# Optimization experiments

Hardware: AMD Instinct MI355X
Metric: run time of the kernel (lower is better)

The kernel has to match this reference:

```python
import jax, jax.numpy as jnp
import numpy as np

B, D = 128, 64  # batch; channel == height == width == dim == 64 (hardcoded by the module)


def setup_inputs() -> dict:
    key = jax.random.key(0)
    kx, kc, kh, kw = jax.random.split(key, 4)
    x = jax.random.normal(kx, (B, D, D, D), dtype=jnp.float32)
    # Stacked 1x1 conv weights: [i (loop index), out_channels, in_channels]
    Wc = jax.random.normal(kc, (D, D, D), dtype=jnp.float32) * 0.1
    Wh = jax.random.normal(kh, (D, D, D), dtype=jnp.float32) * 0.1
    Ww = jax.random.normal(kw, (D, D, D), dtype=jnp.float32) * 0.1
    return {"x": x, "Wc": Wc, "Wh": Wh, "Ww": Ww}


def reference(x, Wc, Wh, Ww):
    # x: [b, c, h, w] with c == h == w == 64
    # Adaptive avg-pool to 1x1 on three permutations -> three [b, 64] vectors.
    c_vec = x.mean(axis=(2, 3))  # pool over (h, w): channel descriptor   [b, 64]
    h_vec = x.mean(axis=(1, 2))  # pool over (c, h): width descriptor    [b, 64]
    w_vec = x.mean(axis=(1, 3))  # pool over (c, w): height descriptor   [b, 64]

    # All 64 per-iteration 1x1 convs + sigmoid as one batched GEMM per branch.
    # Wc[i, o, j]: weight of the i-th conv; conv(C)[o] = sum_j Wc[i,o,j] * c_vec[b,j]
    fc = jax.nn.sigmoid(jnp.einsum('ioj,bj->bio', Wc, c_vec))  # [b, 64(i), 64]
    fh = jax.nn.sigmoid(jnp.einsum('ioj,bj->bio', Wh, h_vec))  # [b, 64(i), 64]
    fw = jax.nn.sigmoid(jnp.einsum('ioj,bj->bio', Ww, w_vec))  # [b, 64(i), 64]

    # recon: bmm(bmm(C, H), W) == outer product fc_i (x) fh_i (x) fw_i, summed over i.
    LR = jnp.einsum('bic,bip,biq->bcpq', fc, fh, fw)  # [b, 64, 64, 64]
    return LR
```

## Files before the change

### kernel.cpp

```cpp
#include <hip/hip_runtime.h>
#include <hip/hip_bf16.h>


#define NB 128

typedef __attribute__((ext_vector_type(8))) short bf16x8;
typedef __attribute__((ext_vector_type(4))) float f32x4;

__device__ __forceinline__ float bf2f(short s) {
    return __uint_as_float(((unsigned)(unsigned short)s) << 16);
}
__device__ __forceinline__ unsigned packbf2(float a, float b) {
    unsigned ua = __float_as_uint(a); ua += 0x7fffu + ((ua >> 16) & 1u);
    unsigned ub = __float_as_uint(b); ub += 0x7fffu + ((ub >> 16) & 1u);
    return (ua >> 16) | (ub & 0xffff0000u);
}
__device__ __forceinline__ unsigned short f2bf(float f) {
    unsigned u = __float_as_uint(f); u += 0x7fffu + ((u >> 16) & 1u);
    return (unsigned short)(u >> 16);
}

__global__ __launch_bounds__(256) void pool_kernel(const float* __restrict__ x,
                                                   float* __restrict__ cvecT,
                                                   float* __restrict__ hv_part,
                                                   float* __restrict__ wv_part)
{
    const int blk  = blockIdx.x;
    const int b    = blk >> 3;
    const int cblk = blk & 7;
    const int t    = threadIdx.x;
    const int wv   = t >> 6;
    const int l    = t & 63;
    const int lg   = l >> 4;
    const int lw   = l & 15;

    __shared__ float cpart[8][4];
    __shared__ float hsum_l[64];
    __shared__ float wpart[4][64];

    const float* xb = x + (size_t)b * 262144 + (size_t)cblk * 32768;

    float cs[8];
    float acc_h[4] = {0.f, 0.f, 0.f, 0.f};
    float acc_w[4] = {0.f, 0.f, 0.f, 0.f};

#pragma unroll
    for (int cc = 0; cc < 8; ++cc) {
        const float* xc = xb + cc * 4096 + wv * 1024 + 4 * l;
        float sc = 0.f;
#pragma unroll
        for (int k = 0; k < 4; ++k) {
            float4 v = *reinterpret_cast<const float4*>(xc + k * 256);
            float s = (v.x + v.y) + (v.z + v.w);
            sc += s;
            acc_h[k] += s;
            acc_w[0] += v.x; acc_w[1] += v.y; acc_w[2] += v.z; acc_w[3] += v.w;
        }
        cs[cc] = sc;
    }

#pragma unroll
    for (int cc = 0; cc < 8; ++cc) {
        float v = cs[cc];
#pragma unroll
        for (int off = 32; off >= 1; off >>= 1) v += __shfl_xor(v, off, 64);
        if (l == 0) cpart[cc][wv] = v;
    }
#pragma unroll
    for (int k = 0; k < 4; ++k) {
        float v = acc_h[k];
        v += __shfl_xor(v, 1, 64);
        v += __shfl_xor(v, 2, 64);
        v += __shfl_xor(v, 4, 64);
        v += __shfl_xor(v, 8, 64);
        if (lw == 0) hsum_l[wv * 16 + k * 4 + lg] = v;
    }
#pragma unroll
    for (int m = 0; m < 4; ++m) {
        float v = acc_w[m];
        v += __shfl_xor(v, 16, 64);
        v += __shfl_xor(v, 32, 64);
        if (lg == 0) wpart[wv][lw * 4 + m] = v;
    }
    __syncthreads();

    const float scale = 1.f / 4096.f;
    if (t < 8) {
        float s = cpart[t][0] + cpart[t][1] + cpart[t][2] + cpart[t][3];
        cvecT[(cblk * 8 + t) * NB + b] = s * scale;
    }
    if (t < 64) {
        wv_part[(cblk * 64 + t) * NB + b] = hsum_l[t] * scale;
        float ws_ = wpart[0][t] + wpart[1][t] + wpart[2][t] + wpart[3][t];
        hv_part[(cblk * 64 + t) * NB + b] = ws_ * scale;
    }
}

__global__ __launch_bounds__(256) void fvec_kernel(const float* __restrict__ Wc,
                                                   const float* __restrict__ Wh,
                                                   const float* __restrict__ Ww,
                                                   const float* __restrict__ cvecT,
                                                   const float* __restrict__ hv_part,
                                                   const float* __restrict__ wv_part,
                                                   unsigned short* __restrict__ fcT,
                                                   unsigned short* __restrict__ fhT,
                                                   unsigned short* __restrict__ fwT)
{
    const int br = blockIdx.x >> 6;
    const int i  = blockIdx.x & 63;
    const float* W = (br == 0) ? Wc : (br == 1) ? Wh : Ww;
    const float* V = (br == 0) ? cvecT : (br == 1) ? hv_part : wv_part;
    unsigned short* outT = (br == 0) ? fcT : (br == 1) ? fhT : fwT;

    __shared__ float Wt[64][64];
    __shared__ float vl[64 * NB];

    const int t = threadIdx.x;
    {
        const float* Wi = W + (size_t)i * 4096;
#pragma unroll
        for (int r = 0; r < 4; ++r) {
            int f = t + 256 * r;
            float4 v = reinterpret_cast<const float4*>(Wi)[f];
            int o = (4 * f) >> 6;
            int j = (4 * f) & 63;
            Wt[j + 0][o] = v.x; Wt[j + 1][o] = v.y; Wt[j + 2][o] = v.z; Wt[j + 3][o] = v.w;
        }
    }
#pragma unroll
    for (int r = 0; r < 8; ++r) {
        int f = t + 256 * r;
        float4 v = reinterpret_cast<const float4*>(V)[f];
        if (br != 0) {
#pragma unroll
            for (int k = 1; k < 8; ++k) {
                float4 u = reinterpret_cast<const float4*>(V + 8192 * k)[f];
                v.x += u.x; v.y += u.y; v.z += u.z; v.w += u.w;
            }
        }
        reinterpret_cast<float4*>(vl)[f] = v;
    }
    __syncthreads();

    const int og = t & 7;
    const int bg = t >> 3;
    const int o0 = og * 8;
    const int b0 = bg * 4;

    float acc[4][8];
#pragma unroll
    for (int bb = 0; bb < 4; ++bb)
#pragma unroll
        for (int oo = 0; oo < 8; ++oo) acc[bb][oo] = 0.f;

#pragma unroll 4
    for (int j = 0; j < 64; ++j) {
        float4 vb = *reinterpret_cast<const float4*>(&vl[j * NB + b0]);
        float4 w0 = *reinterpret_cast<const float4*>(&Wt[j][o0]);
        float4 w1 = *reinterpret_cast<const float4*>(&Wt[j][o0 + 4]);
        float vb_[4] = {vb.x, vb.y, vb.z, vb.w};
        float wv_[8] = {w0.x, w0.y, w0.z, w0.w, w1.x, w1.y, w1.z, w1.w};
#pragma unroll
        for (int bb = 0; bb < 4; ++bb)
#pragma unroll
            for (int oo = 0; oo < 8; ++oo)
                acc[bb][oo] += vb_[bb] * wv_[oo];
    }

#pragma unroll
    for (int bb = 0; bb < 4; ++bb)
#pragma unroll
        for (int oo = 0; oo < 8; ++oo) {
            float sg = 1.f / (1.f + __expf(-acc[bb][oo]));
            outT[((size_t)(b0 + bb) * 64 + (o0 + oo)) * 64 + i] = f2bf(sg);
        }
}

__global__ __launch_bounds__(256) void recon_kernel(const unsigned short* __restrict__ fcT,
                                                    const unsigned short* __restrict__ fhT,
                                                    const unsigned short* __restrict__ fwT,
                                                    float* __restrict__ out)
{
    const int blk  = blockIdx.x;
    const int b    = blk >> 2;
    const int pblk = blk & 3;
    const int t    = threadIdx.x;
    const int w    = t >> 6;
    const int l    = t & 63;
    const int lr   = l & 15;
    const int lg4  = l >> 4;

    __shared__ __align__(16) unsigned short fcl[64 * 72];
    __shared__ __align__(16) unsigned short fwl[64 * 72];
    __shared__ __align__(16) unsigned short fhl[16 * 72];
    __shared__ __align__(16) float bounce[4][16 * 72];

    const unsigned short* fcb = fcT + (size_t)b * 4096;
    const unsigned short* fwb = fwT + (size_t)b * 4096;
    const unsigned short* fhb = fhT + (size_t)b * 4096 + pblk * 1024;

#pragma unroll
    for (int r = 0; r < 2; ++r) {
        int f = t + 256 * r;
        *reinterpret_cast<int4*>(&fcl[(f >> 3) * 72 + (f & 7) * 8]) =
            reinterpret_cast<const int4*>(fcb)[f];
        *reinterpret_cast<int4*>(&fwl[(f >> 3) * 72 + (f & 7) * 8]) =
            reinterpret_cast<const int4*>(fwb)[f];
    }
    if (t < 128) {
        *reinterpret_cast<int4*>(&fhl[(t >> 3) * 72 + (t & 7) * 8]) =
            reinterpret_cast<const int4*>(fhb)[t];
    }
    __syncthreads();

    bf16x8 afr[4][2], wfr[4][2];
#pragma unroll
    for (int ct = 0; ct < 4; ++ct)
#pragma unroll
        for (int kb = 0; kb < 2; ++kb) {
            afr[ct][kb] = *reinterpret_cast<const bf16x8*>(
                &fcl[(ct * 16 + lr) * 72 + kb * 32 + lg4 * 8]);
            wfr[ct][kb] = *reinterpret_cast<const bf16x8*>(
                &fwl[(ct * 16 + lr) * 72 + kb * 32 + lg4 * 8]);
        }

    float* bw = &bounce[w][0];

    for (int pp = 0; pp < 4; ++pp) {
        const int p = w * 4 + pp;
        float hv[16];
#pragma unroll
        for (int kb = 0; kb < 2; ++kb) {
            bf16x8 hf = *reinterpret_cast<const bf16x8*>(
                &fhl[p * 72 + kb * 32 + lg4 * 8]);
#pragma unroll
            for (int j = 0; j < 8; ++j) hv[kb * 8 + j] = bf2f(hf[j]);
        }
        bf16x8 b0s[4], b1s[4];
#pragma unroll
        for (int qt = 0; qt < 4; ++qt) {
            union { unsigned u[4]; bf16x8 v; } bu0, bu1;
#pragma unroll
            for (int jj = 0; jj < 4; ++jj) {
                float p0 = hv[2 * jj]     * bf2f(wfr[qt][0][2 * jj]);
                float p1 = hv[2 * jj + 1] * bf2f(wfr[qt][0][2 * jj + 1]);
                bu0.u[jj] = packbf2(p0, p1);
                float p2 = hv[8 + 2 * jj]     * bf2f(wfr[qt][1][2 * jj]);
                float p3 = hv[8 + 2 * jj + 1] * bf2f(wfr[qt][1][2 * jj + 1]);
                bu1.u[jj] = packbf2(p2, p3);
            }
            b0s[qt] = bu0.v; b1s[qt] = bu1.v;
        }

#pragma unroll
        for (int ct = 0; ct < 4; ++ct) {
            f32x4 acc[4];
#pragma unroll
            for (int qt = 0; qt < 4; ++qt) {
                f32x4 a = {0.f, 0.f, 0.f, 0.f};
                a = __builtin_amdgcn_mfma_f32_16x16x32_bf16(afr[ct][0], b0s[qt], a, 0, 0, 0);
                a = __builtin_amdgcn_mfma_f32_16x16x32_bf16(afr[ct][1], b1s[qt], a, 0, 0, 0);
                acc[qt] = a;
            }
#pragma unroll
            for (int qt = 0; qt < 4; ++qt)
#pragma unroll
                for (int r = 0; r < 4; ++r)
                    bw[(lg4 * 4 + r) * 72 + ((qt * 16 + lr) ^ (lg4 << 4))] = acc[qt][r];
#pragma unroll
            for (int i = 0; i < 4; ++i) {
                int cr = 4 * i + lg4;
                float4 v = *reinterpret_cast<const float4*>(
                    &bw[cr * 72 + ((4 * lr) ^ (i << 4))]);
                *reinterpret_cast<float4*>(
                    out + (((size_t)b * 64 + ct * 16 + cr) * 64 + pblk * 16 + p) * 64 + 4 * lr) = v;
            }
        }
    }
}

extern "C" void kernel_launch(void* const* d_in, const int* in_sizes, int n_in,
                              void* d_out, int out_size, void* d_ws, size_t ws_size,
                              hipStream_t stream) {
    (void)in_sizes; (void)n_in; (void)out_size; (void)ws_size;
    const float* x  = (const float*)d_in[0];
    const float* Wc = (const float*)d_in[1];
    const float* Wh = (const float*)d_in[2];
    const float* Ww = (const float*)d_in[3];
    float* out = (float*)d_out;

    float* ws      = (float*)d_ws;
    float* cvecT   = ws;
    float* hv_part = ws + 8192;
    float* wv_part = ws + 73728;
    unsigned short* fcT = (unsigned short*)(ws + 139264);
    unsigned short* fhT = fcT + 524288;
    unsigned short* fwT = fhT + 524288;

    pool_kernel<<<1024, 256, 0, stream>>>(x, cvecT, hv_part, wv_part);
    fvec_kernel<<<192, 256, 0, stream>>>(Wc, Wh, Ww, cvecT, hv_part, wv_part, fcT, fhT, fwT);
    recon_kernel<<<512, 256, 0, stream>>>(fcT, fhT, fwT, out);
}
```

Measured before the change: 70.86 us.

## Restructure recon GEMM to fold c into B operand and drop LDS bounce

The recon kernel now splits each batch across blocks by channel quarter instead of by p quarter. For each channel it forms the elementwise product fc*fh as the B operand and uses fw as the A operand, so each MFMA tile maps directly onto contiguous q in the output. Results are written straight from accumulators as float4 stores, which removes the shared-memory bounce buffer and its extra LDS traffic and syncless transposes. The trade-off is more VALU work building B fragments (16 per channel) and possibly less coalesced global stores, since each lane writes 16 bytes with rows spread across p.

Result: no change. 70.98 us (+0.2%).

```diff
diff --git a/kernel.cpp b/kernel.cpp
--- a/kernel.cpp
+++ b/kernel.cpp
@@ -181,101 +181,92 @@
                                                     const unsigned short* __restrict__ fwT,
                                                     float* __restrict__ out)
 {
-    const int blk  = blockIdx.x;
-    const int b    = blk >> 2;
-    const int pblk = blk & 3;
-    const int t    = threadIdx.x;
-    const int w    = t >> 6;
-    const int l    = t & 63;
-    const int lr   = l & 15;
-    const int lg4  = l >> 4;
-
-    __shared__ __align__(16) unsigned short fcl[64 * 72];
+    const int blk = blockIdx.x;
+    const int b   = blk >> 2;
+    const int cq  = blk & 3;
+    const int t   = threadIdx.x;
+    const int w   = t >> 6;
+    const int l   = t & 63;
+    const int lr  = l & 15;
+    const int lg4 = l >> 4;
+
+    __shared__ __align__(16) unsigned short fhl[64 * 72];
     __shared__ __align__(16) unsigned short fwl[64 * 72];
-    __shared__ __align__(16) unsigned short fhl[16 * 72];
-    __shared__ __align__(16) float bounce[4][16 * 72];
-
-    const unsigned short* fcb = fcT + (size_t)b * 4096;
+    __shared__ __align__(16) unsigned short fcl[16 * 72];
+
+    const unsigned short* fhb = fhT + (size_t)b * 4096;
     const unsigned short* fwb = fwT + (size_t)b * 4096;
-    const unsigned short* fhb = fhT + (size_t)b * 4096 + pblk * 1024;
+    const unsigned short* fcb = fcT + (size_t)b * 4096 + cq * 1024;
 
 #pragma unroll
     for (int r = 0; r < 2; ++r) {
         int f = t + 256 * r;
-        *reinterpret_cast<int4*>(&fcl[(f >> 3) * 72 + (f & 7) * 8]) =
-            reinterpret_cast<const int4*>(fcb)[f];
+        *reinterpret_cast<int4*>(&fhl[(f >> 3) * 72 + (f & 7) * 8]) =
+            reinterpret_cast<const int4*>(fhb)[f];
         *reinterpret_cast<int4*>(&fwl[(f >> 3) * 72 + (f & 7) * 8]) =
             reinterpret_cast<const int4*>(fwb)[f];
     }
     if (t < 128) {
-        *reinterpret_cast<int4*>(&fhl[(t >> 3) * 72 + (t & 7) * 8]) =
-            reinterpret_cast<const int4*>(fhb)[t];
+        *reinterpret_cast<int4*>(&fcl[(t >> 3) * 72 + (t & 7) * 8]) =
+            reinterpret_cast<const int4*>(fcb)[t];
     }
     __syncthreads();
 
-    bf16x8 afr[4][2], wfr[4][2];
-#pragma unroll
-    for (int ct = 0; ct < 4; ++ct)
+    bf16x8 afw[4][2];
+#pragma unroll
+    for (int qt = 0; qt < 4; ++qt)
+#pragma unroll
+        for (int kb = 0; kb < 2; ++kb)
+            afw[qt][kb] = *reinterpret_cast<const bf16x8*>(
+                &fwl[(qt * 16 + lr) * 72 + kb * 32 + lg4 * 8]);
+
+    float hvf[4][2][8];
+#pragma unroll
+    for (int pt = 0; pt < 4; ++pt)
 #pragma unroll
         for (int kb = 0; kb < 2; ++kb) {
-            afr[ct][kb] = *reinterpret_cast<const bf16x8*>(
-                &fcl[(ct * 16 + lr) * 72 + kb * 32 + lg4 * 8]);
-            wfr[ct][kb] = *reinterpret_cast<const bf16x8*>(
-                &fwl[(ct * 16 + lr) * 72 + kb * 32 + lg4 * 8]);
-        }
-
-    float* bw = &bounce[w][0];
-
-    for (int pp = 0; pp < 4; ++pp) {
-        const int p = w * 4 + pp;
-        float hv[16];
+            bf16x8 h = *reinterpret_cast<const bf16x8*>(
+                &fhl[(pt * 16 + lr) * 72 + kb * 32 + lg4 * 8]);
+#pragma unroll
+            for (int j = 0; j < 8; ++j) hvf[pt][kb][j] = bf2f(h[j]);
+        }
+
+    for (int cc = 0; cc < 4; ++cc) {
+        const int cl = w * 4 + cc;
+        float cvf[16];
 #pragma unroll
         for (int kb = 0; kb < 2; ++kb) {
-            bf16x8 hf = *reinterpret_cast<const bf16x8*>(
-                &fhl[p * 72 + kb * 32 + lg4 * 8]);
-#pragma unroll
-            for (int j = 0; j < 8; ++j) hv[kb * 8 + j] = bf2f(hf[j]);
-        }
-        bf16x8 b0s[4], b1s[4];
-#pragma unroll
-        for (int qt = 0; qt < 4; ++qt) {
-            union { unsigned u[4]; bf16x8 v; } bu0, bu1;
-#pragma unroll
-            for (int jj = 0; jj < 4; ++jj) {
-                float p0 = hv[2 * jj]     * bf2f(wfr[qt][0][2 * jj]);
-                float p1 = hv[2 * jj + 1] * bf2f(wfr[qt][0][2 * jj + 1]);
-                bu0.u[jj] = packbf2(p0, p1);
-                float p2 = hv[8 + 2 * jj]     * bf2f(wfr[qt][1][2 * jj]);
-                float p3 = hv[8 + 2 * jj + 1] * bf2f(wfr[qt][1][2 * jj + 1]);
-                bu1.u[jj] = packbf2(p2, p3);
+            bf16x8 cf = *reinterpret_cast<const bf16x8*>(
+                &fcl[cl * 72 + kb * 32 + lg4 * 8]);
+#pragma unroll
+            for (int j = 0; j < 8; ++j) cvf[kb * 8 + j] = bf2f(cf[j]);
+        }
+        bf16x8 bp[4][2];
+#pragma unroll
+        for (int pt = 0; pt < 4; ++pt)
+#pragma unroll
+            for (int kb = 0; kb < 2; ++kb) {
+                union { unsigned u[4]; bf16x8 v; } bu;
+#pragma unroll
+                for (int jj = 0; jj < 4; ++jj) {
+                    float p0 = cvf[kb * 8 + 2 * jj]     * hvf[pt][kb][2 * jj];
+                    float p1 = cvf[kb * 8 + 2 * jj + 1] * hvf[pt][kb][2 * jj + 1];
+                    bu.u[jj] = packbf2(p0, p1);
+                }
+                bp[pt][kb] = bu.v;
             }
-            b0s[qt] = bu0.v; b1s[qt] = bu1.v;
-        }
-
-#pragma unroll
-        for (int ct = 0; ct < 4; ++ct) {
-            f32x4 acc[4];
+        float* oc = out + (((size_t)b * 64 + cq * 16 + cl) * 64) * 64;
+#pragma unroll
+        for (int pt = 0; pt < 4; ++pt)
 #pragma unroll
             for (int qt = 0; qt < 4; ++qt) {
                 f32x4 a = {0.f, 0.f, 0.f, 0.f};
-                a = __builtin_amdgcn_mfma_f32_16x16x32_bf16(afr[ct][0], b0s[qt], a, 0, 0, 0);
-                a = __builtin_amdgcn_mfma_f32_16x16x32_bf16(afr[ct][1], b1s[qt], a, 0, 0, 0);
-                acc[qt] = a;
+                a = __builtin_amdgcn_mfma_f32_16x16x32_bf16(afw[qt][0], bp[pt][0], a, 0, 0, 0);
+                a = __builtin_amdgcn_mfma_f32_16x16x32_bf16(afw[qt][1], bp[pt][1], a, 0, 0, 0);
+                float4 v; v.x = a[0]; v.y = a[1]; v.z = a[2]; v.w = a[3];
+                *reinterpret_cast<float4*>(
+                    oc + ((size_t)(pt * 16 + lr) * 64) + qt * 16 + lg4 * 4) = v;
             }
-#pragma unroll
-            for (int qt = 0; qt < 4; ++qt)
-#pragma unroll
-                for (int r = 0; r < 4; ++r)
-                    bw[(lg4 * 4 + r) * 72 + ((qt * 16 + lr) ^ (lg4 << 4))] = acc[qt][r];
-#pragma unroll
-            for (int i = 0; i < 4; ++i) {
-                int cr = 4 * i + lg4;
-                float4 v = *reinterpret_cast<const float4*>(
-                    &bw[cr * 72 + ((4 * lr) ^ (i << 4))]);
-                *reinterpret_cast<float4*>(
-                    out + (((size_t)b * 64 + ct * 16 + cr) * 64 + pblk * 16 + p) * 64 + 4 * lr) = v;
-            }
-        }
     }
 }
 
```
